# Kernel optimization log

Measured on AMD Instinct MI355X. Metric: run time of the kernel, lower is better.

The kernel has to match this reference:

```python
import jax, jax.numpy as jnp
import numpy as np

N_NODES = 50000
N_EDGES = 800000
IN_DIM = 128
HID_DIM = 64
OUT_DIM = 40
N_REL = 8


def setup_inputs() -> dict:
    key = jax.random.key(0)
    ks = jax.random.split(key, 12)
    x = jax.random.normal(ks[0], (N_NODES, IN_DIM), dtype=jnp.float32)
    edge_index = jax.random.randint(ks[1], (2, N_EDGES), 0, N_NODES, dtype=jnp.int64)
    edge_type = jax.random.randint(ks[2], (N_EDGES,), 0, N_REL, dtype=jnp.int64)
    s = 0.05
    W1 = jax.random.normal(ks[3], (N_REL, IN_DIM, HID_DIM), dtype=jnp.float32) * s
    root1 = jax.random.normal(ks[4], (IN_DIM, HID_DIM), dtype=jnp.float32) * s
    b1 = jnp.zeros((HID_DIM,), dtype=jnp.float32)
    W2 = jax.random.normal(ks[5], (N_REL, HID_DIM, HID_DIM), dtype=jnp.float32) * s
    root2 = jax.random.normal(ks[6], (HID_DIM, HID_DIM), dtype=jnp.float32) * s
    b2 = jnp.zeros((HID_DIM,), dtype=jnp.float32)
    Wl = jax.random.normal(ks[7], (HID_DIM, OUT_DIM), dtype=jnp.float32) * s
    bl = jnp.zeros((OUT_DIM,), dtype=jnp.float32)
    return {"x": x, "edge_index": edge_index, "edge_type": edge_type,
            "W1": W1, "root1": root1, "b1": b1,
            "W2": W2, "root2": root2, "b2": b2,
            "Wl": Wl, "bl": bl}


def _rgcn_conv(x, W, Wroot, b, src, dst, edge_type):
    # PyG RGCNConv (no bases/blocks, aggr='mean'):
    #   out[i] = sum_r mean_{(j->i) of rel r} (x[j] @ W[r]) + x[i] @ Wroot + b
    N = x.shape[0]
    R = W.shape[0]
    h = jnp.einsum('ni,rio->rno', x, W)        # [R, N, out]
    msgs = h[edge_type, src]                   # [E, out] edge gather
    seg = edge_type * N + dst                  # per (relation, dst) segment
    sums = jax.ops.segment_sum(msgs, seg, num_segments=R * N)
    cnt = jax.ops.segment_sum(jnp.ones((msgs.shape[0],), x.dtype), seg,
                              num_segments=R * N)
    mean = sums / jnp.maximum(cnt, 1.0)[:, None]
    agg = mean.reshape(R, N, -1).sum(axis=0)   # sum over relations
    return agg + x @ Wroot + b


def reference(x, edge_index, edge_type, W1, root1, b1, W2, root2, b2, Wl, bl):
    src, dst = edge_index[0], edge_index[1]
    h = jax.nn.relu(_rgcn_conv(x, W1, root1, b1, src, dst, edge_type))
    # dropout is identity in eval mode
    h = jax.nn.relu(_rgcn_conv(h, W2, root2, b2, src, dst, edge_type))
    logits = h @ Wl + bl
    return jax.nn.log_softmax(logits, axis=1)
```

## Files before the change

### kernel.cpp

```cpp
#include <hip/hip_runtime.h>
#include <hip/hip_bf16.h>
#include <cmath>

#define IN_DIM 128
#define HID 64
#define OUT_DIM 40
#define NREL 8
#define NCOLS 576
#define CAP 64

typedef __attribute__((ext_vector_type(8))) short short8;
typedef __attribute__((ext_vector_type(4))) short short4v;
typedef __attribute__((ext_vector_type(4))) float floatx4;

static __device__ __forceinline__ short f2bf(float f) {
  __hip_bfloat16 h = __float2bfloat16(f);
  return __builtin_bit_cast(short, h);
}
static __device__ __forceinline__ float bflo(unsigned int u) {
  return __int_as_float(u << 16);
}
static __device__ __forceinline__ float bfhi(unsigned int u) {
  return __int_as_float(u & 0xffff0000u);
}
static __device__ __forceinline__ unsigned int packbf(float x, float y) {
  unsigned int lo = (unsigned short)f2bf(x);
  unsigned int hi = (unsigned short)f2bf(y);
  return lo | (hi << 16);
}

__global__ void pack_scatter(const float* __restrict__ W1, const float* __restrict__ root1,
                             short* __restrict__ Bt1,
                             const float* __restrict__ W2, const float* __restrict__ root2,
                             short* __restrict__ Bt2,
                             const int* __restrict__ src, const int* __restrict__ dst,
                             const int* __restrict__ et,
                             int* __restrict__ cursor, int* __restrict__ ev, int E) {
  const int PB1 = (NCOLS * IN_DIM + 255) / 256;
  const int PB2 = (NCOLS * HID + 255) / 256;
  int b = blockIdx.x;
  if (b < PB1) {
    int i = b * 256 + threadIdx.x;
    if (i >= NCOLS * IN_DIM) return;
    int c = i / IN_DIM, k = i % IN_DIM;
    float v = (c < NREL * HID)
      ? W1[((size_t)(c >> 6) * IN_DIM + k) * HID + (c & 63)]
      : root1[(size_t)k * HID + (c - NREL * HID)];
    Bt1[i] = f2bf(v);
  } else if (b < PB1 + PB2) {
    int i = (b - PB1) * 256 + threadIdx.x;
    if (i >= NCOLS * HID) return;
    int c = i / HID, k = i % HID;
    float v = (c < NREL * HID)
      ? W2[((size_t)(c >> 6) * HID + k) * HID + (c & 63)]
      : root2[(size_t)k * HID + (c - NREL * HID)];
    Bt2[i] = f2bf(v);
  } else {
    int e = (b - PB1 - PB2) * 256 + threadIdx.x;
    if (e >= E) return;
    int d = dst[e];
    int pos = atomicAdd(&cursor[d], 1);
    if (pos < CAP)
      __builtin_nontemporal_store((src[e] << 3) | et[e], &ev[d * CAP + pos]);
  }
}

template<int K, int AMODE>
__device__ __forceinline__ void gemm_dev(
    short* As, short* Bs,
    const void* __restrict__ Aptr, const short* __restrict__ Bt,
    const float* __restrict__ bias, short* __restrict__ H,
    unsigned short* __restrict__ AGG, int M, int row0)
{
  constexpr int AST = K + 8;
  int tid = threadIdx.x;
  int wv = tid >> 6, lane = tid & 63;
  int lm = lane & 15, quad = lane >> 4;

  if (AMODE == 0) {
    const float* A = (const float*)Aptr;
    constexpr int CH = K / 4;
    for (int i = tid; i < 64 * CH; i += 256) {
      int r = i / CH, kq = i % CH;
      int gr = row0 + r; if (gr >= M) gr = M - 1;
      float4 v = *(const float4*)(A + (unsigned)(gr * K + kq * 4));
      short4v s;
      s.x = f2bf(v.x); s.y = f2bf(v.y); s.z = f2bf(v.z); s.w = f2bf(v.w);
      *(short4v*)(As + r * AST + kq * 4) = s;
    }
  } else {
    const short* A = (const short*)Aptr;
    constexpr int CH = K / 8;
    for (int i = tid; i < 64 * CH; i += 256) {
      int r = i / CH, ko = i % CH;
      int gr = row0 + r; if (gr >= M) gr = M - 1;
      short8 v = *(const short8*)(A + (unsigned)(gr * K + ko * 8));
      #pragma unroll
      for (int j = 0; j < 8; ++j)
        if ((unsigned short)v[j] & 0x8000u) v[j] = 0;
      *(short8*)(As + r * AST + ko * 8) = v;
    }
  }

  const short* ap = As + (16 * wv + lm) * AST + quad * 8;

  for (int cy = 0; cy < 9; ++cy) {
    constexpr int CB = K / 8;
    for (int i = tid; i < 64 * CB; i += 256) {
      int n = i / CB, ko = i % CB;
      short8 v = *(const short8*)(Bt + (unsigned)((cy * 64 + n) * K + ko * 8));
      *(short8*)(Bs + n * AST + ko * 8) = v;
    }
    __syncthreads();

    floatx4 acc[4] = {{0,0,0,0},{0,0,0,0},{0,0,0,0},{0,0,0,0}};
    #pragma unroll
    for (int ks = 0; ks < K / 32; ++ks) {
      short8 a = *(const short8*)(ap + ks * 32);
      #pragma unroll
      for (int nb = 0; nb < 4; ++nb) {
        short8 b = *(const short8*)(Bs + (nb * 16 + lm) * AST + ks * 32 + quad * 8);
        acc[nb] = __builtin_amdgcn_mfma_f32_16x16x32_bf16(a, b, acc[nb], 0, 0, 0);
      }
    }
    __syncthreads();

    int mbase = row0 + 16 * wv + quad * 4;
    if (cy < 8) {
      #pragma unroll
      for (int nb = 0; nb < 4; ++nb) {
        int col = cy * 64 + nb * 16 + lm;
        #pragma unroll
        for (int r = 0; r < 4; ++r) {
          int mg = mbase + r;
          if (mg < M) H[(unsigned)mg * (NREL * HID) + col] = f2bf(acc[nb][r]);
        }
      }
    } else {
      #pragma unroll
      for (int nb = 0; nb < 4; ++nb) {
        int col = nb * 16 + lm;
        float bv = bias[col];
        #pragma unroll
        for (int r = 0; r < 4; ++r) {
          int mg = mbase + r;
          if (mg < M)
            AGG[(unsigned)mg * HID + col] = (unsigned short)f2bf(acc[nb][r] + bv);
        }
      }
    }
  }
}

__global__ __launch_bounds__(256, 4) void gemm1_mfma(
    const float* __restrict__ A, const short* __restrict__ Bt,
    const float* __restrict__ bias, short* __restrict__ H,
    unsigned short* __restrict__ AGG, int M)
{
  constexpr int AST = IN_DIM + 8;
  __shared__ short As[64 * AST];
  __shared__ short Bs[64 * AST];
  gemm_dev<IN_DIM, 0>(As, Bs, A, Bt, bias, H, AGG, M, blockIdx.x * 64);
}

__global__ __launch_bounds__(256, 4) void gemm2_mfma(
    const unsigned short* __restrict__ A, const short* __restrict__ Bt,
    const float* __restrict__ bias, short* __restrict__ H,
    unsigned short* __restrict__ AGG, int M)
{
  constexpr int AST = HID + 8;
  __shared__ short As[64 * AST];
  __shared__ short Bs[64 * AST];
  gemm_dev<HID, 1>(As, Bs, A, Bt, bias, H, AGG, M, blockIdx.x * 64);
}

static __device__ __forceinline__ void agg_core(
    const uint2* __restrict__ Hu2, const int* __restrict__ evrow,
    int cnt, int lane, int q, int sub,
    float& a0, float& a1, float& a2, float& a3)
{
  int ew = evrow[lane];
  int t = ew & 7;
  float wt = 0.f;
  #pragma unroll
  for (int r = 0; r < 8; ++r) {
    unsigned long long m = __ballot(lane < cnt && t == r);
    int c = __popcll(m);
    if (t == r) wt = 1.0f / (float)(c > 1 ? c : 1);
  }
  int npass = (cnt + 31) >> 5;
  for (int P = 0; P < npass; ++P) {
    int base = P * 32 + q * 8;
    int ee[8]; float ww[8];
    #pragma unroll
    for (int i = 0; i < 8; ++i) {
      int j = base + i;
      int jj = j < cnt ? j : cnt - 1;
      ee[i] = __shfl(ew, jj, 64);
      float w = __shfl(wt, jj, 64);
      ww[i] = (j < cnt) ? w : 0.f;
    }
    uint2 hv[8];
    #pragma unroll
    for (int i = 0; i < 8; ++i)
      hv[i] = Hu2[(unsigned)ee[i] * 16u + (unsigned)sub];
    #pragma unroll
    for (int i = 0; i < 8; ++i) {
      a0 += bflo(hv[i].x) * ww[i];
      a1 += bfhi(hv[i].x) * ww[i];
      a2 += bflo(hv[i].y) * ww[i];
      a3 += bfhi(hv[i].y) * ww[i];
    }
  }
  a0 += __shfl_xor(a0, 16, 64); a0 += __shfl_xor(a0, 32, 64);
  a1 += __shfl_xor(a1, 16, 64); a1 += __shfl_xor(a1, 32, 64);
  a2 += __shfl_xor(a2, 16, 64); a2 += __shfl_xor(a2, 32, 64);
  a3 += __shfl_xor(a3, 16, 64); a3 += __shfl_xor(a3, 32, 64);
}

__global__ __launch_bounds__(256) void csr_agg(
    const short* __restrict__ H, const int* __restrict__ cursor,
    const int* __restrict__ ev, unsigned short* __restrict__ AGG, int N)
{
  int d = blockIdx.x * 4 + (threadIdx.x >> 6);
  if (d >= N) return;
  int lane = threadIdx.x & 63;
  int q = lane >> 4, sub = lane & 15;
  int cnt = cursor[d]; if (cnt > CAP) cnt = CAP;
  float a0 = 0.f, a1 = 0.f, a2 = 0.f, a3 = 0.f;
  uint2* aggrow = (uint2*)(AGG + (size_t)d * HID);
  if (q == 0) {
    uint2 iv = aggrow[sub];
    a0 = bflo(iv.x); a1 = bfhi(iv.x); a2 = bflo(iv.y); a3 = bfhi(iv.y);
  }
  if (cnt > 0)
    agg_core((const uint2*)H, ev + d * CAP, cnt, lane, q, sub, a0, a1, a2, a3);
  if (q == 0) {
    uint2 ov;
    ov.x = packbf(a0, a1);
    ov.y = packbf(a2, a3);
    aggrow[sub] = ov;
  }
}

__global__ __launch_bounds__(256) void csr_agg_final(
    const short* __restrict__ H, const int* __restrict__ cursor,
    const int* __restrict__ ev, const unsigned short* __restrict__ AGG,
    const float* __restrict__ Wl, const float* __restrict__ bl,
    float* __restrict__ out, int N)
{
  __shared__ float sWl[HID * OUT_DIM];
  __shared__ float sbl[OUT_DIM];
  __shared__ float sh[4][HID];
  int tid = threadIdx.x;
  for (int i = tid; i < HID * OUT_DIM; i += 256) sWl[i] = Wl[i];
  if (tid < OUT_DIM) sbl[tid] = bl[tid];
  __syncthreads();

  int wv = tid >> 6, lane = tid & 63;
  int q = lane >> 4, sub = lane & 15;
  int d = blockIdx.x * 4 + wv;
  bool valid = d < N;
  int dc = valid ? d : (N - 1);

  int cnt = cursor[dc]; if (cnt > CAP) cnt = CAP;
  float a0 = 0.f, a1 = 0.f, a2 = 0.f, a3 = 0.f;
  if (q == 0) {
    uint2 iv = ((const uint2*)(AGG + (size_t)dc * HID))[sub];
    a0 = bflo(iv.x); a1 = bfhi(iv.x); a2 = bflo(iv.y); a3 = bfhi(iv.y);
  }
  if (cnt > 0)
    agg_core((const uint2*)H, ev + dc * CAP, cnt, lane, q, sub, a0, a1, a2, a3);
  if (q == 0) {
    float4 v;
    v.x = fmaxf(a0, 0.f); v.y = fmaxf(a1, 0.f);
    v.z = fmaxf(a2, 0.f); v.w = fmaxf(a3, 0.f);
    *(float4*)(&sh[wv][4 * sub]) = v;
  }
  __syncthreads();

  float logit = -__builtin_inff();
  if (lane < OUT_DIM) {
    float t = sbl[lane];
    #pragma unroll 8
    for (int k = 0; k < HID; ++k) t += sh[wv][k] * sWl[k * OUT_DIM + lane];
    logit = t;
  }
  float m = logit;
  #pragma unroll
  for (int o = 32; o > 0; o >>= 1) m = fmaxf(m, __shfl_xor(m, o, 64));
  float ex = (lane < OUT_DIM) ? expf(logit - m) : 0.f;
  float s = ex;
  #pragma unroll
  for (int o = 32; o > 0; o >>= 1) s += __shfl_xor(s, o, 64);
  if (valid && lane < OUT_DIM)
    out[(size_t)d * OUT_DIM + lane] = logit - m - logf(s);
}

extern "C" void kernel_launch(void* const* d_in, const int* in_sizes, int n_in,
                              void* d_out, int out_size, void* d_ws, size_t ws_size,
                              hipStream_t stream) {
  const float* x     = (const float*)d_in[0];
  const int*   eidx  = (const int*)d_in[1];
  const int*   etype = (const int*)d_in[2];
  const float* W1    = (const float*)d_in[3];
  const float* root1 = (const float*)d_in[4];
  const float* b1    = (const float*)d_in[5];
  const float* W2    = (const float*)d_in[6];
  const float* root2 = (const float*)d_in[7];
  const float* b2    = (const float*)d_in[8];
  const float* Wl    = (const float*)d_in[9];
  const float* bl    = (const float*)d_in[10];

  int N = in_sizes[0] / IN_DIM;
  int E = in_sizes[2];
  const int* srcp = eidx;
  const int* dstp = eidx + E;

  char* ws = (char*)d_ws;
  size_t off = 0;
  auto alloc = [&](size_t bytes) -> char* {
    char* p = ws + off;
    off += (bytes + 255) & ~(size_t)255;
    return p;
  };
  short* Bt1    = (short*)alloc((size_t)NCOLS * IN_DIM * 2);
  short* Bt2    = (short*)alloc((size_t)NCOLS * HID * 2);
  int*   cursor = (int*)alloc((size_t)N * 4);
  int*   ev     = (int*)alloc((size_t)N * CAP * 4);
  short* H      = (short*)alloc((size_t)N * NREL * HID * 2);
  unsigned short* AGG1 = (unsigned short*)alloc((size_t)N * HID * 2);
  unsigned short* AGG2 = (unsigned short*)alloc((size_t)N * HID * 2);

  hipMemsetAsync(cursor, 0, (size_t)N * 4, stream);

  const int PB1 = (NCOLS * IN_DIM + 255) / 256;
  const int PB2 = (NCOLS * HID + 255) / 256;
  int SB = (E + 255) / 256;
  pack_scatter<<<PB1 + PB2 + SB, 256, 0, stream>>>(W1, root1, Bt1, W2, root2, Bt2,
                                                   srcp, dstp, etype, cursor, ev, E);

  int GB = (N + 63) / 64;
  gemm1_mfma<<<GB, 256, 0, stream>>>(x, Bt1, b1, H, AGG1, N);
  csr_agg<<<(N + 3) / 4, 256, 0, stream>>>(H, cursor, ev, AGG1, N);
  gemm2_mfma<<<GB, 256, 0, stream>>>(AGG1, Bt2, b2, H, AGG2, N);
  csr_agg_final<<<(N + 3) / 4, 256, 0, stream>>>(H, cursor, ev, AGG2,
                                                 Wl, bl, (float*)d_out, N);
}
```

Baseline: 265.7 us.

## Fuse edge scatter into gemm1 launch, pad cursor counters, vectorize aggregation FMAs

The edge-bucketing scatter moves out of the weight-pack kernel and into the gemm1 launch as extra blocks, so atomic scatter work overlaps with the MFMA GEMM instead of running serially before it. The cursor memset is replaced by zeroing blocks in the pack kernel. Per-node cursors are padded to a 16-int stride so atomics on neighbouring nodes land in separate cache lines. The aggregation inner loop uses 2-wide float vectors to encourage packed FMA. The trade-off is a 16x larger cursor array to zero and sparser cursor reads in the aggregation kernels.

```diff
diff --git a/kernel.cpp b/kernel.cpp
--- a/kernel.cpp
+++ b/kernel.cpp
@@ -8,10 +8,12 @@
 #define NREL 8
 #define NCOLS 576
 #define CAP 64
+#define CSTR 16
 
 typedef __attribute__((ext_vector_type(8))) short short8;
 typedef __attribute__((ext_vector_type(4))) short short4v;
 typedef __attribute__((ext_vector_type(4))) float floatx4;
+typedef __attribute__((ext_vector_type(2))) float f32x2;
 
 static __device__ __forceinline__ short f2bf(float f) {
   __hip_bfloat16 h = __float2bfloat16(f);
@@ -29,13 +31,11 @@
   return lo | (hi << 16);
 }
 
-__global__ void pack_scatter(const float* __restrict__ W1, const float* __restrict__ root1,
-                             short* __restrict__ Bt1,
-                             const float* __restrict__ W2, const float* __restrict__ root2,
-                             short* __restrict__ Bt2,
-                             const int* __restrict__ src, const int* __restrict__ dst,
-                             const int* __restrict__ et,
-                             int* __restrict__ cursor, int* __restrict__ ev, int E) {
+__global__ void pack_zero(const float* __restrict__ W1, const float* __restrict__ root1,
+                          short* __restrict__ Bt1,
+                          const float* __restrict__ W2, const float* __restrict__ root2,
+                          short* __restrict__ Bt2,
+                          int4* __restrict__ curv, int nz) {
   const int PB1 = (NCOLS * IN_DIM + 255) / 256;
   const int PB2 = (NCOLS * HID + 255) / 256;
   int b = blockIdx.x;
@@ -56,12 +56,8 @@
       : root2[(size_t)k * HID + (c - NREL * HID)];
     Bt2[i] = f2bf(v);
   } else {
-    int e = (b - PB1 - PB2) * 256 + threadIdx.x;
-    if (e >= E) return;
-    int d = dst[e];
-    int pos = atomicAdd(&cursor[d], 1);
-    if (pos < CAP)
-      __builtin_nontemporal_store((src[e] << 3) | et[e], &ev[d * CAP + pos]);
+    int i = (b - PB1 - PB2) * 256 + threadIdx.x;
+    if (i < nz) curv[i] = make_int4(0, 0, 0, 0);
   }
 }
 
@@ -152,15 +148,27 @@
   }
 }
 
-__global__ __launch_bounds__(256, 4) void gemm1_mfma(
+__global__ __launch_bounds__(256, 4) void gemm1_scatter(
     const float* __restrict__ A, const short* __restrict__ Bt,
     const float* __restrict__ bias, short* __restrict__ H,
-    unsigned short* __restrict__ AGG, int M)
+    unsigned short* __restrict__ AGG, int M, int GB,
+    const int* __restrict__ src, const int* __restrict__ dst,
+    const int* __restrict__ et,
+    int* __restrict__ cursor, int* __restrict__ ev, int E)
 {
   constexpr int AST = IN_DIM + 8;
   __shared__ short As[64 * AST];
   __shared__ short Bs[64 * AST];
-  gemm_dev<IN_DIM, 0>(As, Bs, A, Bt, bias, H, AGG, M, blockIdx.x * 64);
+  if ((int)blockIdx.x < GB) {
+    gemm_dev<IN_DIM, 0>(As, Bs, A, Bt, bias, H, AGG, M, blockIdx.x * 64);
+  } else {
+    int e = (blockIdx.x - GB) * 256 + threadIdx.x;
+    if (e >= E) return;
+    int d = dst[e];
+    int pos = atomicAdd(&cursor[d * CSTR], 1);
+    if (pos < CAP)
+      __builtin_nontemporal_store((src[e] << 3) | et[e], &ev[d * CAP + pos]);
+  }
 }
 
 __global__ __launch_bounds__(256, 4) void gemm2_mfma(
@@ -188,6 +196,7 @@
     int c = __popcll(m);
     if (t == r) wt = 1.0f / (float)(c > 1 ? c : 1);
   }
+  f32x2 A01 = {a0, a1}, A23 = {a2, a3};
   int npass = (cnt + 31) >> 5;
   for (int P = 0; P < npass; ++P) {
     int base = P * 32 + q * 8;
@@ -206,12 +215,14 @@
       hv[i] = Hu2[(unsigned)ee[i] * 16u + (unsigned)sub];
     #pragma unroll
     for (int i = 0; i < 8; ++i) {
-      a0 += bflo(hv[i].x) * ww[i];
-      a1 += bfhi(hv[i].x) * ww[i];
-      a2 += bflo(hv[i].y) * ww[i];
-      a3 += bfhi(hv[i].y) * ww[i];
-    }
-  }
+      f32x2 w2 = {ww[i], ww[i]};
+      f32x2 h01 = {bflo(hv[i].x), bfhi(hv[i].x)};
+      f32x2 h23 = {bflo(hv[i].y), bfhi(hv[i].y)};
+      A01 += h01 * w2;
+      A23 += h23 * w2;
+    }
+  }
+  a0 = A01.x; a1 = A01.y; a2 = A23.x; a3 = A23.y;
   a0 += __shfl_xor(a0, 16, 64); a0 += __shfl_xor(a0, 32, 64);
   a1 += __shfl_xor(a1, 16, 64); a1 += __shfl_xor(a1, 32, 64);
   a2 += __shfl_xor(a2, 16, 64); a2 += __shfl_xor(a2, 32, 64);
@@ -226,7 +237,7 @@
   if (d >= N) return;
   int lane = threadIdx.x & 63;
   int q = lane >> 4, sub = lane & 15;
-  int cnt = cursor[d]; if (cnt > CAP) cnt = CAP;
+  int cnt = cursor[d * CSTR]; if (cnt > CAP) cnt = CAP;
   float a0 = 0.f, a1 = 0.f, a2 = 0.f, a3 = 0.f;
   uint2* aggrow = (uint2*)(AGG + (size_t)d * HID);
   if (q == 0) {
@@ -263,7 +274,7 @@
   bool valid = d < N;
   int dc = valid ? d : (N - 1);
 
-  int cnt = cursor[dc]; if (cnt > CAP) cnt = CAP;
+  int cnt = cursor[dc * CSTR]; if (cnt > CAP) cnt = CAP;
   float a0 = 0.f, a1 = 0.f, a2 = 0.f, a3 = 0.f;
   if (q == 0) {
     uint2 iv = ((const uint2*)(AGG + (size_t)dc * HID))[sub];
@@ -326,22 +337,24 @@
   };
   short* Bt1    = (short*)alloc((size_t)NCOLS * IN_DIM * 2);
   short* Bt2    = (short*)alloc((size_t)NCOLS * HID * 2);
-  int*   cursor = (int*)alloc((size_t)N * 4);
+  int*   cursor = (int*)alloc((size_t)N * CSTR * 4);
   int*   ev     = (int*)alloc((size_t)N * CAP * 4);
   short* H      = (short*)alloc((size_t)N * NREL * HID * 2);
   unsigned short* AGG1 = (unsigned short*)alloc((size_t)N * HID * 2);
   unsigned short* AGG2 = (unsigned short*)alloc((size_t)N * HID * 2);
 
-  hipMemsetAsync(cursor, 0, (size_t)N * 4, stream);
-
   const int PB1 = (NCOLS * IN_DIM + 255) / 256;
   const int PB2 = (NCOLS * HID + 255) / 256;
+  int nz = N * CSTR / 4;
+  int ZB = (nz + 255) / 256;
+  pack_zero<<<PB1 + PB2 + ZB, 256, 0, stream>>>(W1, root1, Bt1, W2, root2, Bt2,
+                                                (int4*)cursor, nz);
+
+  int GB = (N + 63) / 64;
   int SB = (E + 255) / 256;
-  pack_scatter<<<PB1 + PB2 + SB, 256, 0, stream>>>(W1, root1, Bt1, W2, root2, Bt2,
-                                                   srcp, dstp, etype, cursor, ev, E);
-
-  int GB = (N + 63) / 64;
-  gemm1_mfma<<<GB, 256, 0, stream>>>(x, Bt1, b1, H, AGG1, N);
+  gemm1_scatter<<<GB + SB, 256, 0, stream>>>(x, Bt1, b1, H, AGG1, N, GB,
+                                             srcp, dstp, etype, cursor, ev, E);
+
   csr_agg<<<(N + 3) / 4, 256, 0, stream>>>(H, cursor, ev, AGG1, N);
   gemm2_mfma<<<GB, 256, 0, stream>>>(AGG1, Bt2, b2, H, AGG2, N);
   csr_agg_final<<<(N + 3) / 4, 256, 0, stream>>>(H, cursor, ev, AGG2,
```

New measurement: 233.3 us. -12.2%, faster.
